# Kernel optimization log

Hardware: AMD Instinct MI355X
Metric: run time of the kernel (lower is better)

Reference implementation:

```python
import jax, jax.numpy as jnp
import numpy as np

N_NODES = 100000
N_EDGES = 800000
IN_FEATS = 128
HIDDEN = 64
SCALE = 0.5 ** 0.5  # sqrt(0.5) residual scale
BN_EPS = 1e-5


def setup_inputs() -> dict:
    key = jax.random.key(0)
    ks = jax.random.split(key, 12)
    return {
        "src": jax.random.randint(ks[0], (N_EDGES,), 0, N_NODES, dtype=jnp.int64)
        if jax.config.jax_enable_x64 else jax.random.randint(ks[0], (N_EDGES,), 0, N_NODES),
        "dst": jax.random.randint(ks[1], (N_EDGES,), 0, N_NODES),
        "x": jax.random.normal(ks[2], (N_NODES, IN_FEATS), dtype=jnp.float32),
        "fc_w": jax.random.normal(ks[3], (IN_FEATS, HIDDEN), dtype=jnp.float32) * 0.05,
        "fc_b": jax.random.normal(ks[4], (HIDDEN,), dtype=jnp.float32) * 0.05,
        "w1": jax.random.normal(ks[5], (HIDDEN, HIDDEN), dtype=jnp.float32) * 0.05,
        "b1": jax.random.normal(ks[6], (HIDDEN,), dtype=jnp.float32) * 0.05,
        "w2": jax.random.normal(ks[7], (HIDDEN, HIDDEN), dtype=jnp.float32) * 0.05,
        "b2": jax.random.normal(ks[8], (HIDDEN,), dtype=jnp.float32) * 0.05,
        "gamma": jax.random.normal(ks[9], (HIDDEN,), dtype=jnp.float32) * 0.05 + 1.0,
        "beta": jax.random.normal(ks[10], (HIDDEN,), dtype=jnp.float32) * 0.05,
    }


def _graph_conv(h, w, b, src, dst, norm_src, norm_dst, n_nodes):
    # DGL GraphConv, norm='both': y = D_in^{-1/2} A D_out^{-1/2} (h W) + b
    h = h @ w                                   # [N, H]
    m = h[src] * norm_src[:, None]              # gather + src-degree norm, [E, H]
    agg = jax.ops.segment_sum(m, dst, num_segments=n_nodes)  # scatter-add, [N, H]
    return agg * norm_dst[:, None] + b


def reference(src, dst, x, fc_w, fc_b, w1, b1, w2, b2, gamma, beta):
    n_nodes = x.shape[0]
    ones_e = jnp.ones(src.shape[0], dtype=x.dtype)
    deg_out = jnp.clip(jax.ops.segment_sum(ones_e, src, num_segments=n_nodes), 1.0)
    deg_in = jnp.clip(jax.ops.segment_sum(ones_e, dst, num_segments=n_nodes), 1.0)
    norm_src = (deg_out ** -0.5)[src]           # per-edge source normalization
    norm_dst = deg_in ** -0.5                   # per-node destination normalization

    h = x @ fc_w + fc_b                          # fc: [N, H]
    h = (h + _graph_conv(h, w1, b1, src, dst, norm_src, norm_dst, n_nodes)) * SCALE
    h = (h + _graph_conv(h, w2, b2, src, dst, norm_src, norm_dst, n_nodes)) * SCALE

    # BatchNorm1d (training-mode batch statistics over nodes, biased variance)
    mu = h.mean(axis=0)
    var = ((h - mu) ** 2).mean(axis=0)
    h = (h - mu) * jax.lax.rsqrt(var + BN_EPS) * gamma + beta
    return h
```

## Files before the change

kernel.cpp:

```cpp
#include <hip/hip_runtime.h>

#define HIDDEN 64
#define INFEAT 128
#define SCALE_C 0.70710678118654752f
#define BN_EPS 1e-5f
#define AGG_GRID 2048
#define RED_BLK 32

__device__ __forceinline__ int rli(int v, int l){ return __builtin_amdgcn_readlane(v, l); }
__device__ __forceinline__ float rlf(float v, int l){
  return __int_as_float(__builtin_amdgcn_readlane(__float_as_int(v), l));
}

template<int KDIM, bool ADDB, bool FUSET>
__device__ __forceinline__ void gemm_body(int bid, const float* __restrict__ X,
    const float* __restrict__ W, const float* __restrict__ B,
    float* __restrict__ Y, const float* __restrict__ W2, float* __restrict__ T, int N)
{
  __shared__ float smem[64 * 65];
  const int tid  = threadIdx.x;
  const int lane = tid & 63;
  const int wid  = __builtin_amdgcn_readfirstlane(tid >> 6);
  const int c0 = wid * 16;
  const int base = bid * 64;
  const int gnode = base + lane;

  float acc[16];
  #pragma unroll
  for (int c = 0; c < 16; ++c) acc[c] = ADDB ? B[c0 + c] : 0.f;

  constexpr int NCHUNK = KDIM / 32;
  #pragma unroll 1
  for (int ck = 0; ck < NCHUNK; ++ck){
    __syncthreads();
    #pragma unroll
    for (int i = 0; i < 2; ++i){
      int f  = i * 256 + tid;
      int nd = f >> 3;
      int kq = f & 7;
      float4 v = make_float4(0.f, 0.f, 0.f, 0.f);
      if (base + nd < N)
        v = *(const float4*)(X + (size_t)(base + nd) * KDIM + ck * 32 + kq * 4);
      float* p = &smem[nd * 65 + kq * 4];
      p[0] = v.x; p[1] = v.y; p[2] = v.z; p[3] = v.w;
    }
    __syncthreads();
    const float* wrow = W + (size_t)ck * 32 * HIDDEN + c0;
    #pragma unroll
    for (int k = 0; k < 32; ++k){
      float xv = smem[lane * 65 + k];
      #pragma unroll
      for (int c = 0; c < 16; ++c)
        acc[c] = fmaf(xv, wrow[k * HIDDEN + c], acc[c]);
    }
  }

  if (gnode < N){
    float4* yp = (float4*)(Y + (size_t)gnode * HIDDEN + c0);
    #pragma unroll
    for (int j = 0; j < 4; ++j)
      yp[j] = make_float4(acc[4*j], acc[4*j+1], acc[4*j+2], acc[4*j+3]);
  }

  if constexpr (FUSET){
    __syncthreads();
    #pragma unroll
    for (int c = 0; c < 16; ++c) smem[lane * 65 + c0 + c] = acc[c];
    __syncthreads();
    float tacc[16];
    #pragma unroll
    for (int c = 0; c < 16; ++c) tacc[c] = 0.f;
    const float* w2r = W2 + c0;
    #pragma unroll
    for (int k = 0; k < 64; ++k){
      float hv = smem[lane * 65 + k];
      #pragma unroll
      for (int c = 0; c < 16; ++c)
        tacc[c] = fmaf(hv, w2r[k * HIDDEN + c], tacc[c]);
    }
    if (gnode < N){
      float4* tp = (float4*)(T + (size_t)gnode * HIDDEN + c0);
      #pragma unroll
      for (int j = 0; j < 4; ++j)
        tp[j] = make_float4(tacc[4*j], tacc[4*j+1], tacc[4*j+2], tacc[4*j+3]);
    }
  }
}

__device__ __forceinline__ int role_gemm_idx(int b, int GB, int TOT, int& histIdx){
  int fb  = (int)(((long)b * GB) / TOT);
  int fb1 = (int)(((long)(b + 1) * GB) / TOT);
  histIdx = b - fb;
  return (fb1 > fb) ? fb : -1;
}

__global__ __launch_bounds__(256) void k_mega1(const int* __restrict__ dst,
    int* __restrict__ degI, int* __restrict__ rank, int E,
    const float* __restrict__ x, const float* __restrict__ fc_w,
    const float* __restrict__ fc_b, float* __restrict__ h,
    const float* __restrict__ w1, float* __restrict__ t, int N, int GB, int TOT){
  int hIdx;
  int g = role_gemm_idx(blockIdx.x, GB, TOT, hIdx);
  if (g >= 0) gemm_body<INFEAT, true, true>(g, x, fc_w, fc_b, h, w1, t, N);
  else {
    int e0 = hIdx * 2048 + threadIdx.x;
    #pragma unroll
    for (int i = 0; i < 8; ++i){
      int e = e0 + i * 256;
      if (e < E) rank[e] = atomicAdd(&degI[dst[e]], 1);
    }
  }
}

__global__ __launch_bounds__(256) void k_place(const int* __restrict__ src,
    const int* __restrict__ dst, const int* __restrict__ rank,
    const int* __restrict__ rp, int* __restrict__ cs, int* __restrict__ degO, int E){
  int e0 = blockIdx.x * 2048 + threadIdx.x;
  #pragma unroll
  for (int i = 0; i < 8; ++i){
    int e = e0 + i * 256;
    if (e < E){
      int s = src[e];
      cs[rp[dst[e]] + rank[e]] = s;
      atomicAdd(&degO[s], 1);
    }
  }
}

__global__ __launch_bounds__(256) void k_gemm64(const float* __restrict__ X,
    const float* __restrict__ W, float* __restrict__ Y, int N){
  gemm_body<HIDDEN, false, false>(blockIdx.x, X, W, nullptr, Y, nullptr, nullptr, N);
}

__global__ void k_scan1(const int* __restrict__ deg, int* __restrict__ bsum, int N){
  __shared__ int sh[256];
  int t = threadIdx.x;
  int i = blockIdx.x * 256 + t;
  sh[t] = (i < N) ? deg[i] : 0;
  __syncthreads();
  for (int ofs = 128; ofs > 0; ofs >>= 1){
    if (t < ofs) sh[t] += sh[t + ofs];
    __syncthreads();
  }
  if (t == 0) bsum[blockIdx.x] = sh[0];
}

__global__ void k_scan2(int* __restrict__ bsum, int NB){
  __shared__ int sh[512];
  int t = threadIdx.x;
  int v = (t < NB) ? bsum[t] : 0;
  sh[t] = v;
  __syncthreads();
  for (int ofs = 1; ofs < 512; ofs <<= 1){
    int u = (t >= ofs) ? sh[t - ofs] : 0;
    __syncthreads();
    sh[t] += u;
    __syncthreads();
  }
  if (t < NB) bsum[t] = sh[t] - v;
}

__global__ void k_scan3(const int* __restrict__ degI, const int* __restrict__ bofs,
                        int* __restrict__ rp, float* __restrict__ norm_in, int N, int E){
  __shared__ int sh[256];
  int t = threadIdx.x;
  int i = blockIdx.x * 256 + t;
  int v = (i < N) ? degI[i] : 0;
  sh[t] = v;
  __syncthreads();
  for (int ofs = 1; ofs < 256; ofs <<= 1){
    int u = (t >= ofs) ? sh[t - ofs] : 0;
    __syncthreads();
    sh[t] += u;
    __syncthreads();
  }
  if (i < N){
    int excl = sh[t] - v + bofs[blockIdx.x];
    rp[i] = excl;
    if (i == N - 1) rp[N] = E;
    norm_in[i] = rsqrtf((float)max(v, 1));
  }
}

template<bool PRE>
__device__ __forceinline__ float4 gather_row4(const int* __restrict__ rp,
    const int* __restrict__ cs, const float* __restrict__ t,
    const int* __restrict__ degO, int n, int g, int s4){
  const int start = rp[n], end = rp[n + 1];
  float4 acc = make_float4(0.f, 0.f, 0.f, 0.f);
  int j = start + g;
  for (; j + 4 < end; j += 8){
    int a0 = cs[j], a1 = cs[j + 4];
    float4 v0 = *(const float4*)(t + (size_t)a0 * HIDDEN + s4);
    float4 v1 = *(const float4*)(t + (size_t)a1 * HIDDEN + s4);
    if (PRE){
      acc.x += v0.x; acc.y += v0.y; acc.z += v0.z; acc.w += v0.w;
      acc.x += v1.x; acc.y += v1.y; acc.z += v1.z; acc.w += v1.w;
    } else {
      float n0 = rsqrtf((float)degO[a0]);
      float n1 = rsqrtf((float)degO[a1]);
      acc.x = fmaf(v0.x, n0, acc.x); acc.y = fmaf(v0.y, n0, acc.y);
      acc.z = fmaf(v0.z, n0, acc.z); acc.w = fmaf(v0.w, n0, acc.w);
      acc.x = fmaf(v1.x, n1, acc.x); acc.y = fmaf(v1.y, n1, acc.y);
      acc.z = fmaf(v1.z, n1, acc.z); acc.w = fmaf(v1.w, n1, acc.w);
    }
  }
  if (j < end){
    int a = cs[j];
    float4 v = *(const float4*)(t + (size_t)a * HIDDEN + s4);
    if (PRE){
      acc.x += v.x; acc.y += v.y; acc.z += v.z; acc.w += v.w;
    } else {
      float nn = rsqrtf((float)degO[a]);
      acc.x = fmaf(v.x, nn, acc.x); acc.y = fmaf(v.y, nn, acc.y);
      acc.z = fmaf(v.z, nn, acc.z); acc.w = fmaf(v.w, nn, acc.w);
    }
  }
  return acc;
}

__device__ __forceinline__ float4 xreduce4(float4 a){
  #pragma unroll
  for (int m = 16; m <= 32; m <<= 1){
    a.x += __shfl_xor(a.x, m, 64);
    a.y += __shfl_xor(a.y, m, 64);
    a.z += __shfl_xor(a.z, m, 64);
    a.w += __shfl_xor(a.w, m, 64);
  }
  return a;
}

template<bool BN, bool PRE, bool FUSET2>
__global__ __launch_bounds__(256, 4) void k_agg(const int* __restrict__ rp, const int* __restrict__ cs,
    const float* __restrict__ t, const int* __restrict__ degO,
    const float* __restrict__ norm_in, const float* __restrict__ b,
    const float* __restrict__ w2, float* __restrict__ h,
    float* __restrict__ t2, float* __restrict__ bnpart, int N)
{
  const int tid  = threadIdx.x;
  const int lane = tid & 63;
  const int g    = lane >> 4;
  const int s    = lane & 15;
  const int s4   = s * 4;
  const int wv = (blockIdx.x * 256 + tid) >> 6;
  const int nw = (gridDim.x * 256) >> 6;
  const float4 bv = ((const float4*)b)[s];
  float4 s1 = make_float4(0.f,0.f,0.f,0.f), s2 = make_float4(0.f,0.f,0.f,0.f);

  __shared__ float w2l[FUSET2 ? (HIDDEN * HIDDEN) : 1];
  if constexpr (FUSET2){
    for (int i = tid; i < HIDDEN * HIDDEN; i += 256) w2l[i] = w2[i];
    __syncthreads();
  }

  for (int n = wv; n < N; n += nw){
    float4 acc = gather_row4<PRE>(rp, cs, t, degO, n, g, s4);
    acc = xreduce4(acc);
    const size_t rowo = (size_t)n * HIDDEN;
    const float4 hv = *(const float4*)(h + rowo + s4);
    const float ni = norm_in[n];
    float4 v;
    v.x = (hv.x + acc.x * ni + bv.x) * SCALE_C;
    v.y = (hv.y + acc.y * ni + bv.y) * SCALE_C;
    v.z = (hv.z + acc.z * ni + bv.z) * SCALE_C;
    v.w = (hv.w + acc.w * ni + bv.w) * SCALE_C;
    if (g == 0){
      *(float4*)(h + rowo + s4) = v;
      if (BN){
        s1.x += v.x; s1.y += v.y; s1.z += v.z; s1.w += v.w;
        s2.x += v.x*v.x; s2.y += v.y*v.y; s2.z += v.z*v.z; s2.w += v.w*v.w;
      }
    }
    if constexpr (FUSET2){
      float nout = rsqrtf((float)max(degO[n], 1));
      float ta0 = 0.f, ta1 = 0.f, ta2 = 0.f, ta3 = 0.f;
      #pragma unroll
      for (int k = 0; k < 64; k += 4){
        const int ln = k >> 2;
        ta0 = fmaf(rlf(v.x, ln), w2l[(k    ) * HIDDEN + lane], ta0);
        ta1 = fmaf(rlf(v.y, ln), w2l[(k + 1) * HIDDEN + lane], ta1);
        ta2 = fmaf(rlf(v.z, ln), w2l[(k + 2) * HIDDEN + lane], ta2);
        ta3 = fmaf(rlf(v.w, ln), w2l[(k + 3) * HIDDEN + lane], ta3);
      }
      t2[rowo + lane] = ((ta0 + ta1) + (ta2 + ta3)) * nout;
    }
  }

  if (BN){
    __shared__ float l1[4][64], l2[4][64];
    const int wid = tid >> 6;
    if (g == 0){
      l1[wid][s4+0] = s1.x; l1[wid][s4+1] = s1.y; l1[wid][s4+2] = s1.z; l1[wid][s4+3] = s1.w;
      l2[wid][s4+0] = s2.x; l2[wid][s4+1] = s2.y; l2[wid][s4+2] = s2.z; l2[wid][s4+3] = s2.w;
    }
    __syncthreads();
    if (tid < 64){
      float a1 = l1[0][tid] + l1[1][tid] + l1[2][tid] + l1[3][tid];
      float a2 = l2[0][tid] + l2[1][tid] + l2[2][tid] + l2[3][tid];
      bnpart[blockIdx.x * 128 + tid] = a1;
      bnpart[blockIdx.x * 128 + 64 + tid] = a2;
    }
  }
}

__global__ __launch_bounds__(256) void k_bnred(const float* __restrict__ bnpart,
    float* __restrict__ bnred, int nblk){
  int col  = threadIdx.x & 127;
  int half = threadIdx.x >> 7;
  int rows = nblk / RED_BLK;
  int r0 = blockIdx.x * rows;
  float s = 0.f;
  for (int r = half; r < rows; r += 2)
    s += bnpart[(size_t)(r0 + r) * 128 + col];
  __shared__ float sh[256];
  sh[threadIdx.x] = s;
  __syncthreads();
  if (threadIdx.x < 128)
    bnred[blockIdx.x * 128 + threadIdx.x] = sh[threadIdx.x] + sh[threadIdx.x + 128];
}

__global__ void k_bnfin(const float* __restrict__ bnred,
    const float* __restrict__ gamma, const float* __restrict__ beta,
    float* __restrict__ bnab, float invN){
  int c = threadIdx.x;
  float s1 = 0.f, s2 = 0.f;
  #pragma unroll
  for (int b = 0; b < RED_BLK; ++b){ s1 += bnred[b*128 + c]; s2 += bnred[b*128 + 64 + c]; }
  float mu  = s1 * invN;
  float var = s2 * invN - mu * mu;
  float rstd = rsqrtf(var + BN_EPS);
  float sc = gamma[c] * rstd;
  bnab[c] = sc;
  bnab[64 + c] = beta[c] - mu * sc;
}

__global__ void k_bnapply(float* __restrict__ h, const float* __restrict__ bnab, long total4){
  long i = (long)blockIdx.x * blockDim.x + threadIdx.x;
  if (i < total4){
    int c = (int)((i * 4) & 63);
    float4 v = ((float4*)h)[i];
    v.x = fmaf(v.x, bnab[c],     bnab[64 + c]);
    v.y = fmaf(v.y, bnab[c + 1], bnab[65 + c]);
    v.z = fmaf(v.z, bnab[c + 2], bnab[66 + c]);
    v.w = fmaf(v.w, bnab[c + 3], bnab[67 + c]);
    ((float4*)h)[i] = v;
  }
}

extern "C" void kernel_launch(void* const* d_in, const int* in_sizes, int n_in,
                              void* d_out, int out_size, void* d_ws, size_t ws_size,
                              hipStream_t stream){
  const int* src = (const int*)d_in[0];
  const int* dst = (const int*)d_in[1];
  const float* x     = (const float*)d_in[2];
  const float* fc_w  = (const float*)d_in[3];
  const float* fc_b  = (const float*)d_in[4];
  const float* w1    = (const float*)d_in[5];
  const float* b1    = (const float*)d_in[6];
  const float* w2    = (const float*)d_in[7];
  const float* b2    = (const float*)d_in[8];
  const float* gamma = (const float*)d_in[9];
  const float* beta  = (const float*)d_in[10];
  const int E = in_sizes[0];
  const int N = in_sizes[2] / INFEAT;
  const int NB  = (N + 255) / 256;
  const int EB8 = (E + 2047) / 2048;
  const int GB  = (N + 63) / 64;
  const int TOT = EB8 + GB;

  float* h = (float*)d_out;

  const size_t Nh = (size_t)N * HIDDEN;
  size_t need = (2 * Nh + N + (size_t)AGG_GRID * 128 + RED_BLK * 128 + 128) * 4
              + ((size_t)3 * N + 1 + 512 + 2 * (size_t)E) * 4;
  const bool fused = ws_size >= need;

  float* t        = (float*)d_ws;
  float* t2       = fused ? (t + Nh) : nullptr;
  float* norm_in  = fused ? (t2 + Nh) : (t + Nh);
  float* bnpart   = norm_in + N;
  float* bnred    = bnpart + AGG_GRID * 128;
  float* bnab     = bnred + RED_BLK * 128;
  int*   degO     = (int*)(bnab + 128);
  int*   degI     = degO + N;
  int*   rp       = degI + N;
  int*   bsum     = rp + N + 1;
  int*   rank     = bsum + 512;
  int*   cs       = rank + E;

  hipMemsetAsync(degO, 0, 2 * (size_t)N * sizeof(int), stream);

  k_mega1<<<TOT, 256, 0, stream>>>(dst, degI, rank, E,
                                   x, fc_w, fc_b, h, w1, t, N, GB, TOT);

  k_scan1<<<NB, 256, 0, stream>>>(degI, bsum, N);
  k_scan2<<<1, 512, 0, stream>>>(bsum, NB);
  k_scan3<<<NB, 256, 0, stream>>>(degI, bsum, rp, norm_in, N, E);

  k_place<<<EB8, 256, 0, stream>>>(src, dst, rank, rp, cs, degO, E);

  if (fused){
    k_agg<false, false, true><<<AGG_GRID, 256, 0, stream>>>(
        rp, cs, t, degO, norm_in, b1, w2, h, t2, nullptr, N);
    k_agg<true, true, false><<<AGG_GRID, 256, 0, stream>>>(
        rp, cs, t2, degO, norm_in, b2, nullptr, h, nullptr, bnpart, N);
  } else {
    k_agg<false, false, false><<<AGG_GRID, 256, 0, stream>>>(
        rp, cs, t, degO, norm_in, b1, nullptr, h, nullptr, nullptr, N);
    k_gemm64<<<GB, 256, 0, stream>>>(h, w2, t, N);
    k_agg<true, false, false><<<AGG_GRID, 256, 0, stream>>>(
        rp, cs, t, degO, norm_in, b2, nullptr, h, nullptr, bnpart, N);
  }

  k_bnred<<<RED_BLK, 256, 0, stream>>>(bnpart, bnred, AGG_GRID);
  k_bnfin<<<1, 64, 0, stream>>>(bnred, gamma, beta, bnab, 1.0f / (float)N);
  long total4 = (long)N * HIDDEN / 4;
  k_bnapply<<<(int)((total4 + 255) / 256), 256, 0, stream>>>(h, bnab, total4);
}
```

Measured before the change: 343.3 us.

## Store gathered transformed features in bf16 to halve gather traffic

```diff
diff --git a/kernel.cpp b/kernel.cpp
--- a/kernel.cpp
+++ b/kernel.cpp
@@ -7,15 +7,24 @@
 #define AGG_GRID 2048
 #define RED_BLK 32
 
-__device__ __forceinline__ int rli(int v, int l){ return __builtin_amdgcn_readlane(v, l); }
 __device__ __forceinline__ float rlf(float v, int l){
   return __int_as_float(__builtin_amdgcn_readlane(__float_as_int(v), l));
 }
+
+__device__ __forceinline__ unsigned f2bf1(float x){
+  unsigned u = __float_as_uint(x);
+  return (u + 0x7fffu + ((u >> 16) & 1u)) >> 16;
+}
+__device__ __forceinline__ unsigned packbf(float lo, float hi){
+  return f2bf1(lo) | (f2bf1(hi) << 16);
+}
+__device__ __forceinline__ float bflo(unsigned u){ return __uint_as_float(u << 16); }
+__device__ __forceinline__ float bfhi(unsigned u){ return __uint_as_float(u & 0xffff0000u); }
 
 template<int KDIM, bool ADDB, bool FUSET>
 __device__ __forceinline__ void gemm_body(int bid, const float* __restrict__ X,
     const float* __restrict__ W, const float* __restrict__ B,
-    float* __restrict__ Y, const float* __restrict__ W2, float* __restrict__ T, int N)
+    float* __restrict__ Y, const float* __restrict__ W2, unsigned* __restrict__ T, int N)
 {
   __shared__ float smem[64 * 65];
   const int tid  = threadIdx.x;
@@ -79,10 +88,12 @@
         tacc[c] = fmaf(hv, w2r[k * HIDDEN + c], tacc[c]);
     }
     if (gnode < N){
-      float4* tp = (float4*)(T + (size_t)gnode * HIDDEN + c0);
+      unsigned pk[8];
       #pragma unroll
-      for (int j = 0; j < 4; ++j)
-        tp[j] = make_float4(tacc[4*j], tacc[4*j+1], tacc[4*j+2], tacc[4*j+3]);
+      for (int j = 0; j < 8; ++j) pk[j] = packbf(tacc[2*j], tacc[2*j+1]);
+      uint4* tp = (uint4*)(T + (size_t)gnode * 32 + wid * 8);
+      tp[0] = make_uint4(pk[0], pk[1], pk[2], pk[3]);
+      tp[1] = make_uint4(pk[4], pk[5], pk[6], pk[7]);
     }
   }
 }
@@ -98,7 +109,7 @@
     int* __restrict__ degI, int* __restrict__ rank, int E,
     const float* __restrict__ x, const float* __restrict__ fc_w,
     const float* __restrict__ fc_b, float* __restrict__ h,
-    const float* __restrict__ w1, float* __restrict__ t, int N, int GB, int TOT){
+    const float* __restrict__ w1, unsigned* __restrict__ t, int N, int GB, int TOT){
   int hIdx;
   int g = role_gemm_idx(blockIdx.x, GB, TOT, hIdx);
   if (g >= 0) gemm_body<INFEAT, true, true>(g, x, fc_w, fc_b, h, w1, t, N);
@@ -127,11 +138,6 @@
   }
 }
 
-__global__ __launch_bounds__(256) void k_gemm64(const float* __restrict__ X,
-    const float* __restrict__ W, float* __restrict__ Y, int N){
-  gemm_body<HIDDEN, false, false>(blockIdx.x, X, W, nullptr, Y, nullptr, nullptr, N);
-}
-
 __global__ void k_scan1(const int* __restrict__ deg, int* __restrict__ bsum, int N){
   __shared__ int sh[256];
   int t = threadIdx.x;
@@ -184,36 +190,36 @@
 
 template<bool PRE>
 __device__ __forceinline__ float4 gather_row4(const int* __restrict__ rp,
-    const int* __restrict__ cs, const float* __restrict__ t,
-    const int* __restrict__ degO, int n, int g, int s4){
+    const int* __restrict__ cs, const uint2* __restrict__ tb,
+    const int* __restrict__ degO, int n, int g, int s){
   const int start = rp[n], end = rp[n + 1];
   float4 acc = make_float4(0.f, 0.f, 0.f, 0.f);
   int j = start + g;
   for (; j + 4 < end; j += 8){
     int a0 = cs[j], a1 = cs[j + 4];
-    float4 v0 = *(const float4*)(t + (size_t)a0 * HIDDEN + s4);
-    float4 v1 = *(const float4*)(t + (size_t)a1 * HIDDEN + s4);
+    uint2 q0 = tb[(size_t)a0 * 16 + s];
+    uint2 q1 = tb[(size_t)a1 * 16 + s];
     if (PRE){
-      acc.x += v0.x; acc.y += v0.y; acc.z += v0.z; acc.w += v0.w;
-      acc.x += v1.x; acc.y += v1.y; acc.z += v1.z; acc.w += v1.w;
+      acc.x += bflo(q0.x); acc.y += bfhi(q0.x); acc.z += bflo(q0.y); acc.w += bfhi(q0.y);
+      acc.x += bflo(q1.x); acc.y += bfhi(q1.x); acc.z += bflo(q1.y); acc.w += bfhi(q1.y);
     } else {
       float n0 = rsqrtf((float)degO[a0]);
       float n1 = rsqrtf((float)degO[a1]);
-      acc.x = fmaf(v0.x, n0, acc.x); acc.y = fmaf(v0.y, n0, acc.y);
-      acc.z = fmaf(v0.z, n0, acc.z); acc.w = fmaf(v0.w, n0, acc.w);
-      acc.x = fmaf(v1.x, n1, acc.x); acc.y = fmaf(v1.y, n1, acc.y);
-      acc.z = fmaf(v1.z, n1, acc.z); acc.w = fmaf(v1.w, n1, acc.w);
+      acc.x = fmaf(bflo(q0.x), n0, acc.x); acc.y = fmaf(bfhi(q0.x), n0, acc.y);
+      acc.z = fmaf(bflo(q0.y), n0, acc.z); acc.w = fmaf(bfhi(q0.y), n0, acc.w);
+      acc.x = fmaf(bflo(q1.x), n1, acc.x); acc.y = fmaf(bfhi(q1.x), n1, acc.y);
+      acc.z = fmaf(bflo(q1.y), n1, acc.z); acc.w = fmaf(bfhi(q1.y), n1, acc.w);
     }
   }
   if (j < end){
     int a = cs[j];
-    float4 v = *(const float4*)(t + (size_t)a * HIDDEN + s4);
+    uint2 q = tb[(size_t)a * 16 + s];
     if (PRE){
-      acc.x += v.x; acc.y += v.y; acc.z += v.z; acc.w += v.w;
+      acc.x += bflo(q.x); acc.y += bfhi(q.x); acc.z += bflo(q.y); acc.w += bfhi(q.y);
     } else {
       float nn = rsqrtf((float)degO[a]);
-      acc.x = fmaf(v.x, nn, acc.x); acc.y = fmaf(v.y, nn, acc.y);
-      acc.z = fmaf(v.z, nn, acc.z); acc.w = fmaf(v.w, nn, acc.w);
+      acc.x = fmaf(bflo(q.x), nn, acc.x); acc.y = fmaf(bfhi(q.x), nn, acc.y);
+      acc.z = fmaf(bflo(q.y), nn, acc.z); acc.w = fmaf(bfhi(q.y), nn, acc.w);
     }
   }
   return acc;
@@ -232,10 +238,10 @@
 
 template<bool BN, bool PRE, bool FUSET2>
 __global__ __launch_bounds__(256, 4) void k_agg(const int* __restrict__ rp, const int* __restrict__ cs,
-    const float* __restrict__ t, const int* __restrict__ degO,
+    const uint2* __restrict__ t, const int* __restrict__ degO,
     const float* __restrict__ norm_in, const float* __restrict__ b,
     const float* __restrict__ w2, float* __restrict__ h,
-    float* __restrict__ t2, float* __restrict__ bnpart, int N)
+    unsigned* __restrict__ t2, float* __restrict__ bnpart, int N)
 {
   const int tid  = threadIdx.x;
   const int lane = tid & 63;
@@ -247,14 +253,14 @@
   const float4 bv = ((const float4*)b)[s];
   float4 s1 = make_float4(0.f,0.f,0.f,0.f), s2 = make_float4(0.f,0.f,0.f,0.f);
 
-  __shared__ float w2l[FUSET2 ? (HIDDEN * HIDDEN) : 1];
+  float w2c[64];
   if constexpr (FUSET2){
-    for (int i = tid; i < HIDDEN * HIDDEN; i += 256) w2l[i] = w2[i];
-    __syncthreads();
+    #pragma unroll
+    for (int k = 0; k < 64; ++k) w2c[k] = w2[k * HIDDEN + lane];
   }
 
   for (int n = wv; n < N; n += nw){
-    float4 acc = gather_row4<PRE>(rp, cs, t, degO, n, g, s4);
+    float4 acc = gather_row4<PRE>(rp, cs, t, degO, n, g, s);
     acc = xreduce4(acc);
     const size_t rowo = (size_t)n * HIDDEN;
     const float4 hv = *(const float4*)(h + rowo + s4);
@@ -277,12 +283,15 @@
       #pragma unroll
       for (int k = 0; k < 64; k += 4){
         const int ln = k >> 2;
-        ta0 = fmaf(rlf(v.x, ln), w2l[(k    ) * HIDDEN + lane], ta0);
-        ta1 = fmaf(rlf(v.y, ln), w2l[(k + 1) * HIDDEN + lane], ta1);
-        ta2 = fmaf(rlf(v.z, ln), w2l[(k + 2) * HIDDEN + lane], ta2);
-        ta3 = fmaf(rlf(v.w, ln), w2l[(k + 3) * HIDDEN + lane], ta3);
+        ta0 = fmaf(rlf(v.x, ln), w2c[k],     ta0);
+        ta1 = fmaf(rlf(v.y, ln), w2c[k + 1], ta1);
+        ta2 = fmaf(rlf(v.z, ln), w2c[k + 2], ta2);
+        ta3 = fmaf(rlf(v.w, ln), w2c[k + 3], ta3);
       }
-      t2[rowo + lane] = ((ta0 + ta1) + (ta2 + ta3)) * nout;
+      float ta = ((ta0 + ta1) + (ta2 + ta3)) * nout;
+      float tn = __shfl_xor(ta, 1, 64);
+      if ((lane & 1) == 0)
+        t2[rowo / 2 + (lane >> 1)] = packbf(ta, tn);
     }
   }
 
@@ -371,13 +380,9 @@
   float* h = (float*)d_out;
 
   const size_t Nh = (size_t)N * HIDDEN;
-  size_t need = (2 * Nh + N + (size_t)AGG_GRID * 128 + RED_BLK * 128 + 128) * 4
-              + ((size_t)3 * N + 1 + 512 + 2 * (size_t)E) * 4;
-  const bool fused = ws_size >= need;
-
-  float* t        = (float*)d_ws;
-  float* t2       = fused ? (t + Nh) : nullptr;
-  float* norm_in  = fused ? (t2 + Nh) : (t + Nh);
+  unsigned short* tb  = (unsigned short*)d_ws;
+  unsigned short* t2b = tb + Nh;
+  float* norm_in  = (float*)(t2b + Nh);
   float* bnpart   = norm_in + N;
   float* bnred    = bnpart + AGG_GRID * 128;
   float* bnab     = bnred + RED_BLK * 128;
@@ -391,7 +396,7 @@
   hipMemsetAsync(degO, 0, 2 * (size_t)N * sizeof(int), stream);
 
   k_mega1<<<TOT, 256, 0, stream>>>(dst, degI, rank, E,
-                                   x, fc_w, fc_b, h, w1, t, N, GB, TOT);
+                                   x, fc_w, fc_b, h, w1, (unsigned*)tb, N, GB, TOT);
 
   k_scan1<<<NB, 256, 0, stream>>>(degI, bsum, N);
   k_scan2<<<1, 512, 0, stream>>>(bsum, NB);
@@ -399,18 +404,10 @@
 
   k_place<<<EB8, 256, 0, stream>>>(src, dst, rank, rp, cs, degO, E);
 
-  if (fused){
-    k_agg<false, false, true><<<AGG_GRID, 256, 0, stream>>>(
-        rp, cs, t, degO, norm_in, b1, w2, h, t2, nullptr, N);
-    k_agg<true, true, false><<<AGG_GRID, 256, 0, stream>>>(
-        rp, cs, t2, degO, norm_in, b2, nullptr, h, nullptr, bnpart, N);
-  } else {
-    k_agg<false, false, false><<<AGG_GRID, 256, 0, stream>>>(
-        rp, cs, t, degO, norm_in, b1, nullptr, h, nullptr, nullptr, N);
-    k_gemm64<<<GB, 256, 0, stream>>>(h, w2, t, N);
-    k_agg<true, false, false><<<AGG_GRID, 256, 0, stream>>>(
-        rp, cs, t, degO, norm_in, b2, nullptr, h, nullptr, bnpart, N);
-  }
+  k_agg<false, false, true><<<AGG_GRID, 256, 0, stream>>>(
+      rp, cs, (const uint2*)tb, degO, norm_in, b1, w2, h, (unsigned*)t2b, nullptr, N);
+  k_agg<true, true, false><<<AGG_GRID, 256, 0, stream>>>(
+      rp, cs, (const uint2*)t2b, degO, norm_in, b2, nullptr, h, nullptr, bnpart, N);
 
   k_bnred<<<RED_BLK, 256, 0, stream>>>(bnpart, bnred, AGG_GRID);
   k_bnfin<<<1, 64, 0, stream>>>(bnred, gamma, beta, bnab, 1.0f / (float)N);
```

Result: slower. 350.9 us (+2.2%).

## Software-pipeline node aggregation prefetch and keep W2 in registers

Applied to the files above, without the earlier changes.

```diff
diff --git a/kernel.cpp b/kernel.cpp
--- a/kernel.cpp
+++ b/kernel.cpp
@@ -7,7 +7,6 @@
 #define AGG_GRID 2048
 #define RED_BLK 32
 
-__device__ __forceinline__ int rli(int v, int l){ return __builtin_amdgcn_readlane(v, l); }
 __device__ __forceinline__ float rlf(float v, int l){
   return __int_as_float(__builtin_amdgcn_readlane(__float_as_int(v), l));
 }
@@ -127,11 +126,6 @@
   }
 }
 
-__global__ __launch_bounds__(256) void k_gemm64(const float* __restrict__ X,
-    const float* __restrict__ W, float* __restrict__ Y, int N){
-  gemm_body<HIDDEN, false, false>(blockIdx.x, X, W, nullptr, Y, nullptr, nullptr, N);
-}
-
 __global__ void k_scan1(const int* __restrict__ deg, int* __restrict__ bsum, int N){
   __shared__ int sh[256];
   int t = threadIdx.x;
@@ -183,37 +177,27 @@
 }
 
 template<bool PRE>
-__device__ __forceinline__ float4 gather_row4(const int* __restrict__ rp,
-    const int* __restrict__ cs, const float* __restrict__ t,
-    const int* __restrict__ degO, int n, int g, int s4){
-  const int start = rp[n], end = rp[n + 1];
+__device__ __forceinline__ float4 gather_pre(const int* __restrict__ cs,
+    const float* __restrict__ t, const int* __restrict__ degO,
+    int start, int end, int g, int s4, int i0, int i1)
+{
   float4 acc = make_float4(0.f, 0.f, 0.f, 0.f);
-  int j = start + g;
-  for (; j + 4 < end; j += 8){
-    int a0 = cs[j], a1 = cs[j + 4];
-    float4 v0 = *(const float4*)(t + (size_t)a0 * HIDDEN + s4);
-    float4 v1 = *(const float4*)(t + (size_t)a1 * HIDDEN + s4);
-    if (PRE){
-      acc.x += v0.x; acc.y += v0.y; acc.z += v0.z; acc.w += v0.w;
-      acc.x += v1.x; acc.y += v1.y; acc.z += v1.z; acc.w += v1.w;
-    } else {
-      float n0 = rsqrtf((float)degO[a0]);
-      float n1 = rsqrtf((float)degO[a1]);
-      acc.x = fmaf(v0.x, n0, acc.x); acc.y = fmaf(v0.y, n0, acc.y);
-      acc.z = fmaf(v0.z, n0, acc.z); acc.w = fmaf(v0.w, n0, acc.w);
-      acc.x = fmaf(v1.x, n1, acc.x); acc.y = fmaf(v1.y, n1, acc.y);
-      acc.z = fmaf(v1.z, n1, acc.z); acc.w = fmaf(v1.w, n1, acc.w);
-    }
-  }
-  if (j < end){
-    int a = cs[j];
-    float4 v = *(const float4*)(t + (size_t)a * HIDDEN + s4);
-    if (PRE){
-      acc.x += v.x; acc.y += v.y; acc.z += v.z; acc.w += v.w;
-    } else {
-      float nn = rsqrtf((float)degO[a]);
-      acc.x = fmaf(v.x, nn, acc.x); acc.y = fmaf(v.y, nn, acc.y);
-      acc.z = fmaf(v.z, nn, acc.z); acc.w = fmaf(v.w, nn, acc.w);
+  int j0 = start + g;
+  while (j0 < end){
+    const bool b1 = (j0 + 4 < end);
+    const int k1 = b1 ? i1 : i0;
+    const float4 r0 = *(const float4*)(t + (size_t)i0 * HIDDEN + s4);
+    const float4 r1 = *(const float4*)(t + (size_t)k1 * HIDDEN + s4);
+    const float w0 = PRE ? 1.f : rsqrtf((float)degO[i0]);
+    const float w1 = b1 ? (PRE ? 1.f : rsqrtf((float)degO[k1])) : 0.f;
+    acc.x = fmaf(r0.x, w0, acc.x); acc.y = fmaf(r0.y, w0, acc.y);
+    acc.z = fmaf(r0.z, w0, acc.z); acc.w = fmaf(r0.w, w0, acc.w);
+    acc.x = fmaf(r1.x, w1, acc.x); acc.y = fmaf(r1.y, w1, acc.y);
+    acc.z = fmaf(r1.z, w1, acc.z); acc.w = fmaf(r1.w, w1, acc.w);
+    j0 += 8;
+    if (j0 < end){
+      i0 = cs[j0];
+      i1 = (j0 + 4 < end) ? cs[j0 + 4] : i0;
     }
   }
   return acc;
@@ -245,30 +229,54 @@
   const int wv = (blockIdx.x * 256 + tid) >> 6;
   const int nw = (gridDim.x * 256) >> 6;
   const float4 bv = ((const float4*)b)[s];
-  float4 s1 = make_float4(0.f,0.f,0.f,0.f), s2 = make_float4(0.f,0.f,0.f,0.f);
-
-  __shared__ float w2l[FUSET2 ? (HIDDEN * HIDDEN) : 1];
+  float4 s1 = make_float4(0.f,0.f,0.f,0.f), s2v = make_float4(0.f,0.f,0.f,0.f);
+
+  float w2c[64];
   if constexpr (FUSET2){
-    for (int i = tid; i < HIDDEN * HIDDEN; i += 256) w2l[i] = w2[i];
-    __syncthreads();
-  }
-
-  for (int n = wv; n < N; n += nw){
-    float4 acc = gather_row4<PRE>(rp, cs, t, degO, n, g, s4);
+    #pragma unroll
+    for (int k = 0; k < 64; ++k) w2c[k] = w2[k * HIDDEN + lane];
+  }
+
+  int nA = wv;
+  int sA = 0, eA = 0, pA0 = 0, pA1 = 0; float niA = 0.f;
+  float4 hA = make_float4(0.f,0.f,0.f,0.f);
+  if (nA < N){
+    sA = rp[nA]; eA = rp[nA + 1];
+    niA = norm_in[nA];
+    hA = *(const float4*)(h + (size_t)nA * HIDDEN + s4);
+    pA0 = (sA + g < eA) ? cs[sA + g] : 0;
+    pA1 = (sA + g + 4 < eA) ? cs[sA + g + 4] : 0;
+  }
+  int nB = nA + nw;
+  int sB = 0, eB = 0;
+  if (nB < N){ sB = rp[nB]; eB = rp[nB + 1]; }
+
+  for (int n = nA; n < N; n += nw){
+    const int nC = n + 2 * nw;
+    int sC = 0, eC = 0;
+    if (nC < N){ sC = rp[nC]; eC = rp[nC + 1]; }
+    int pB0 = 0, pB1 = 0; float niB = 0.f;
+    float4 hB = make_float4(0.f,0.f,0.f,0.f);
+    if (n + nw < N){
+      pB0 = (sB + g < eB) ? cs[sB + g] : 0;
+      pB1 = (sB + g + 4 < eB) ? cs[sB + g + 4] : 0;
+      niB = norm_in[n + nw];
+      hB = *(const float4*)(h + (size_t)(n + nw) * HIDDEN + s4);
+    }
+
+    float4 acc = gather_pre<PRE>(cs, t, degO, sA, eA, g, s4, pA0, pA1);
     acc = xreduce4(acc);
     const size_t rowo = (size_t)n * HIDDEN;
-    const float4 hv = *(const float4*)(h + rowo + s4);
-    const float ni = norm_in[n];
     float4 v;
-    v.x = (hv.x + acc.x * ni + bv.x) * SCALE_C;
-    v.y = (hv.y + acc.y * ni + bv.y) * SCALE_C;
-    v.z = (hv.z + acc.z * ni + bv.z) * SCALE_C;
-    v.w = (hv.w + acc.w * ni + bv.w) * SCALE_C;
+    v.x = (hA.x + acc.x * niA + bv.x) * SCALE_C;
+    v.y = (hA.y + acc.y * niA + bv.y) * SCALE_C;
+    v.z = (hA.z + acc.z * niA + bv.z) * SCALE_C;
+    v.w = (hA.w + acc.w * niA + bv.w) * SCALE_C;
     if (g == 0){
       *(float4*)(h + rowo + s4) = v;
       if (BN){
         s1.x += v.x; s1.y += v.y; s1.z += v.z; s1.w += v.w;
-        s2.x += v.x*v.x; s2.y += v.y*v.y; s2.z += v.z*v.z; s2.w += v.w*v.w;
+        s2v.x += v.x*v.x; s2v.y += v.y*v.y; s2v.z += v.z*v.z; s2v.w += v.w*v.w;
       }
     }
     if constexpr (FUSET2){
@@ -277,13 +285,15 @@
       #pragma unroll
       for (int k = 0; k < 64; k += 4){
         const int ln = k >> 2;
-        ta0 = fmaf(rlf(v.x, ln), w2l[(k    ) * HIDDEN + lane], ta0);
-        ta1 = fmaf(rlf(v.y, ln), w2l[(k + 1) * HIDDEN + lane], ta1);
-        ta2 = fmaf(rlf(v.z, ln), w2l[(k + 2) * HIDDEN + lane], ta2);
-        ta3 = fmaf(rlf(v.w, ln), w2l[(k + 3) * HIDDEN + lane], ta3);
+        ta0 = fmaf(rlf(v.x, ln), w2c[k],     ta0);
+        ta1 = fmaf(rlf(v.y, ln), w2c[k + 1], ta1);
+        ta2 = fmaf(rlf(v.z, ln), w2c[k + 2], ta2);
+        ta3 = fmaf(rlf(v.w, ln), w2c[k + 3], ta3);
       }
       t2[rowo + lane] = ((ta0 + ta1) + (ta2 + ta3)) * nout;
     }
+    sA = sB; eA = eB; pA0 = pB0; pA1 = pB1; niA = niB; hA = hB;
+    sB = sC; eB = eC;
   }
 
   if (BN){
@@ -291,7 +301,7 @@
     const int wid = tid >> 6;
     if (g == 0){
       l1[wid][s4+0] = s1.x; l1[wid][s4+1] = s1.y; l1[wid][s4+2] = s1.z; l1[wid][s4+3] = s1.w;
-      l2[wid][s4+0] = s2.x; l2[wid][s4+1] = s2.y; l2[wid][s4+2] = s2.z; l2[wid][s4+3] = s2.w;
+      l2[wid][s4+0] = s2v.x; l2[wid][s4+1] = s2v.y; l2[wid][s4+2] = s2v.z; l2[wid][s4+3] = s2v.w;
     }
     __syncthreads();
     if (tid < 64){
@@ -371,13 +381,9 @@
   float* h = (float*)d_out;
 
   const size_t Nh = (size_t)N * HIDDEN;
-  size_t need = (2 * Nh + N + (size_t)AGG_GRID * 128 + RED_BLK * 128 + 128) * 4
-              + ((size_t)3 * N + 1 + 512 + 2 * (size_t)E) * 4;
-  const bool fused = ws_size >= need;
-
   float* t        = (float*)d_ws;
-  float* t2       = fused ? (t + Nh) : nullptr;
-  float* norm_in  = fused ? (t2 + Nh) : (t + Nh);
+  float* t2       = t + Nh;
+  float* norm_in  = t2 + Nh;
   float* bnpart   = norm_in + N;
   float* bnred    = bnpart + AGG_GRID * 128;
   float* bnab     = bnred + RED_BLK * 128;
@@ -399,18 +405,10 @@
 
   k_place<<<EB8, 256, 0, stream>>>(src, dst, rank, rp, cs, degO, E);
 
-  if (fused){
-    k_agg<false, false, true><<<AGG_GRID, 256, 0, stream>>>(
-        rp, cs, t, degO, norm_in, b1, w2, h, t2, nullptr, N);
-    k_agg<true, true, false><<<AGG_GRID, 256, 0, stream>>>(
-        rp, cs, t2, degO, norm_in, b2, nullptr, h, nullptr, bnpart, N);
-  } else {
-    k_agg<false, false, false><<<AGG_GRID, 256, 0, stream>>>(
-        rp, cs, t, degO, norm_in, b1, nullptr, h, nullptr, nullptr, N);
-    k_gemm64<<<GB, 256, 0, stream>>>(h, w2, t, N);
-    k_agg<true, false, false><<<AGG_GRID, 256, 0, stream>>>(
-        rp, cs, t, degO, norm_in, b2, nullptr, h, nullptr, bnpart, N);
-  }
+  k_agg<false, false, true><<<AGG_GRID, 256, 0, stream>>>(
+      rp, cs, t, degO, norm_in, b1, w2, h, t2, nullptr, N);
+  k_agg<true, true, false><<<AGG_GRID, 256, 0, stream>>>(
+      rp, cs, t2, degO, norm_in, b2, nullptr, h, nullptr, bnpart, N);
 
   k_bnred<<<RED_BLK, 256, 0, stream>>>(bnpart, bnred, AGG_GRID);
   k_bnfin<<<1, 64, 0, stream>>>(bnred, gamma, beta, bnab, 1.0f / (float)N);
```

Measured after the change: 332.4 us. 3.2% less time.
